# Performance work log

Measured on AMD Instinct MI355X. Metric: run time of the kernel, lower is better.

## Reference

```python
import jax, jax.numpy as jnp
import numpy as np
import math

B, H, S, D = 4, 16, 2048, 64

def setup_inputs() -> dict:
    key = jax.random.key(0)
    kq, kk, kv = jax.random.split(key, 3)
    Q = jax.random.normal(kq, (B, H, S, D), dtype=jnp.float32)
    K = jax.random.normal(kk, (B, H, S, D), dtype=jnp.float32)
    V = jax.random.normal(kv, (B, H, S, D), dtype=jnp.float32)
    # causal mask, broadcast to [B, H, S, S] as the module expects '... queries keys'
    causal = jnp.tril(jnp.ones((S, S), dtype=bool))
    mask = jnp.broadcast_to(causal, (B, H, S, S))
    return {"Q": Q, "K": K, "V": V, "mask": mask}

def reference(Q, K, V, mask):
    d_k = Q.shape[-1]
    # [B,H,S_q,S_k] scores
    qk = jnp.einsum('bhqd,bhkd->bhqk', Q, K) / math.sqrt(d_k)
    qk = jnp.where(mask, qk, -jnp.inf)
    sm = jax.nn.softmax(qk, axis=-1)
    return jnp.einsum('bhqk,bhkd->bhqd', sm, V)
```

## Files before the change

### kernel.cpp

```cpp
#include <hip/hip_runtime.h>

#define SEQ  2048
#define DH   64
#define QBLK 128
#define KBLK 64
#define NQB  (SEQ/QBLK)
#define NTIL (SEQ/KBLK)
#define THR  11.5f
#define KPAT(r) ((((r)&3)) + 8*((r)>>2))
#define WS_NEEDED ((size_t)2 * 64 * SEQ * DH * 2)

typedef short bf16x8 __attribute__((ext_vector_type(8)));
typedef float f32x16 __attribute__((ext_vector_type(16)));

union V4U { unsigned int w[4]; bf16x8 v; };

__device__ __forceinline__ short bfbits(float f) {
    unsigned int u = __float_as_uint(f);
    u += 0x7fff + ((u >> 16) & 1);
    return (short)(u >> 16);
}
__device__ __forceinline__ unsigned int cvtpk(float lo, float hi) {
    unsigned int r;
    asm("v_cvt_pk_bf16_f32 %0, %1, %2" : "=v"(r) : "v"(lo), "v"(hi));
    return r;
}
__device__ __forceinline__ int swz(int row, int col) {
    return row * 64 + (col ^ ((row & 7) << 3));
}
__device__ __forceinline__ void gload16(const void* g, void* l) {
    __builtin_amdgcn_global_load_lds(
        (const __attribute__((address_space(1))) unsigned int*)g,
        (__attribute__((address_space(3))) unsigned int*)l,
        16, 0, 0);
}

__global__ __launch_bounds__(256) void prep_kv(const float* __restrict__ Kg,
                                               const float* __restrict__ Vg,
                                               short* __restrict__ Kimg,
                                               short* __restrict__ Vimg) {
    __shared__ __align__(16) short Vt[64 * 64];
    const int tid = threadIdx.x;
    const int t   = blockIdx.x & (NTIL - 1);
    const int bh  = blockIdx.x / NTIL;
    const int kb  = t * KBLK;

    const float* Kb = Kg + (size_t)bh * SEQ * DH;
    const float* Vb = Vg + (size_t)bh * SEQ * DH;
    short* kim = Kimg + ((size_t)bh * NTIL + t) * 4096;
    short* vim = Vimg + ((size_t)bh * NTIL + t) * 4096;

    {
        const int kr = tid >> 2, sd0 = (tid & 3) * 16;
        const float* src = Kb + (size_t)(kb + kr) * DH + sd0;
        const float4 a0 = *reinterpret_cast<const float4*>(src);
        const float4 a1 = *reinterpret_cast<const float4*>(src + 4);
        const float4 a2 = *reinterpret_cast<const float4*>(src + 8);
        const float4 a3 = *reinterpret_cast<const float4*>(src + 12);
        V4U u0, u1;
        u0.w[0] = cvtpk(a0.x, a0.y); u0.w[1] = cvtpk(a0.z, a0.w);
        u0.w[2] = cvtpk(a1.x, a1.y); u0.w[3] = cvtpk(a1.z, a1.w);
        u1.w[0] = cvtpk(a2.x, a2.y); u1.w[1] = cvtpk(a2.z, a2.w);
        u1.w[2] = cvtpk(a3.x, a3.y); u1.w[3] = cvtpk(a3.z, a3.w);
        *reinterpret_cast<bf16x8*>(&kim[swz(kr, sd0)])     = u0.v;
        *reinterpret_cast<bf16x8*>(&kim[swz(kr, sd0 + 8)]) = u1.v;
    }
    {
        const int vk = tid & 63, vd0 = (tid >> 6) * 16;
        const float* src = Vb + (size_t)(kb + vk) * DH + vd0;
        const float4 b0 = *reinterpret_cast<const float4*>(src);
        const float4 b1 = *reinterpret_cast<const float4*>(src + 4);
        const float4 b2 = *reinterpret_cast<const float4*>(src + 8);
        const float4 b3 = *reinterpret_cast<const float4*>(src + 12);
        const float vv[16] = {b0.x,b0.y,b0.z,b0.w, b1.x,b1.y,b1.z,b1.w,
                              b2.x,b2.y,b2.z,b2.w, b3.x,b3.y,b3.z,b3.w};
        #pragma unroll
        for (int i = 0; i < 16; ++i)
            Vt[swz(vd0 + i, vk)] = bfbits(vv[i]);
    }
    __syncthreads();
    *reinterpret_cast<bf16x8*>(&vim[tid * 16])     = *reinterpret_cast<const bf16x8*>(&Vt[tid * 16]);
    *reinterpret_cast<bf16x8*>(&vim[tid * 16 + 8]) = *reinterpret_cast<const bf16x8*>(&Vt[tid * 16 + 8]);
}

__device__ __forceinline__ void load_kf8(const short* __restrict__ Ksb, int ql, int h,
                                         bf16x8 (&kf)[8]) {
    #pragma unroll
    for (int dc = 0; dc < 4; ++dc) {
        kf[dc]     = *reinterpret_cast<const bf16x8*>(&Ksb[swz(ql,      dc * 16 + h * 8)]);
        kf[4 + dc] = *reinterpret_cast<const bf16x8*>(&Ksb[swz(32 + ql, dc * 16 + h * 8)]);
    }
}
__device__ __forceinline__ void load_vf8(const short* __restrict__ Vtb, int ql, int h,
                                         bf16x8 (&vf)[8]) {
    #pragma unroll
    for (int kt = 0; kt < 4; ++kt) {
        vf[kt]     = *reinterpret_cast<const bf16x8*>(&Vtb[swz(ql,      kt * 16 + h * 8)]);
        vf[4 + kt] = *reinterpret_cast<const bf16x8*>(&Vtb[swz(32 + ql, kt * 16 + h * 8)]);
    }
}
__device__ __forceinline__ void qk_phase(const bf16x8 (&kf)[8], const bf16x8 (&qb)[4],
                                         f32x16& s0, f32x16& s1, bool v2) {
    #pragma unroll
    for (int i = 0; i < 16; ++i) s0[i] = 0.f;
    __builtin_amdgcn_s_setprio(1);
    #pragma unroll
    for (int dc = 0; dc < 4; ++dc)
        s0 = __builtin_amdgcn_mfma_f32_32x32x16_bf16(kf[dc], qb[dc], s0, 0, 0, 0);
    __builtin_amdgcn_s_setprio(0);
    if (v2) {
        #pragma unroll
        for (int i = 0; i < 16; ++i) s1[i] = 0.f;
        __builtin_amdgcn_s_setprio(1);
        #pragma unroll
        for (int dc = 0; dc < 4; ++dc)
            s1 = __builtin_amdgcn_mfma_f32_32x32x16_bf16(kf[4 + dc], qb[dc], s1, 0, 0, 0);
        __builtin_amdgcn_s_setprio(0);
    }
}
__device__ __forceinline__ void sm_pack(f32x16& s0, f32x16& s1, bool v2,
                                        int kb, int qw, int q, int h,
                                        float& m, float& lsum,
                                        f32x16& o0, f32x16& o1, bf16x8 (&pa)[4]) {
    if (kb + 31 > qw) {
        #pragma unroll
        for (int r = 0; r < 16; ++r)
            if (kb + KPAT(r) + 4 * h > q) s0[r] = -1e30f;
    }
    if (v2 && (kb + 63 > qw)) {
        #pragma unroll
        for (int r = 0; r < 16; ++r)
            if (kb + 32 + KPAT(r) + 4 * h > q) s1[r] = -1e30f;
    }
    float mx = s0[0];
    #pragma unroll
    for (int r = 1; r < 16; ++r) mx = fmaxf(mx, s0[r]);
    if (v2) {
        #pragma unroll
        for (int r = 0; r < 16; ++r) mx = fmaxf(mx, s1[r]);
    }
    if (!__all(mx <= m + THR)) {
        mx = fmaxf(mx, __shfl_xor(mx, 32));
        const float mn  = fmaxf(m, mx);
        const float scl = __builtin_amdgcn_exp2f(m - mn);
        m = mn;
        lsum *= scl;
        #pragma unroll
        for (int r = 0; r < 16; ++r) {
            const float sr = __shfl(scl, KPAT(r) + 4 * h);
            o0[r] *= sr; o1[r] *= sr;
        }
    }
    #pragma unroll
    for (int r = 0; r < 16; ++r) { s0[r] = __builtin_amdgcn_exp2f(s0[r] - m); lsum += s0[r]; }
    #pragma unroll
    for (int oct = 0; oct < 2; ++oct) {
        const unsigned int A0 = cvtpk(s0[oct*8+0], s0[oct*8+1]);
        const unsigned int A1 = cvtpk(s0[oct*8+2], s0[oct*8+3]);
        const unsigned int B0 = cvtpk(s0[oct*8+4], s0[oct*8+5]);
        const unsigned int B1 = cvtpk(s0[oct*8+6], s0[oct*8+7]);
        const unsigned int t0 = h ? A0 : B0, t1 = h ? A1 : B1;
        const unsigned int r0 = (unsigned int)__shfl_xor((int)t0, 32);
        const unsigned int r1 = (unsigned int)__shfl_xor((int)t1, 32);
        V4U u;
        u.w[0] = h ? r0 : A0; u.w[1] = h ? r1 : A1;
        u.w[2] = h ? B0 : r0; u.w[3] = h ? B1 : r1;
        pa[oct] = u.v;
    }
    if (v2) {
        #pragma unroll
        for (int r = 0; r < 16; ++r) { s1[r] = __builtin_amdgcn_exp2f(s1[r] - m); lsum += s1[r]; }
        #pragma unroll
        for (int oct = 0; oct < 2; ++oct) {
            const unsigned int A0 = cvtpk(s1[oct*8+0], s1[oct*8+1]);
            const unsigned int A1 = cvtpk(s1[oct*8+2], s1[oct*8+3]);
            const unsigned int B0 = cvtpk(s1[oct*8+4], s1[oct*8+5]);
            const unsigned int B1 = cvtpk(s1[oct*8+6], s1[oct*8+7]);
            const unsigned int t0 = h ? A0 : B0, t1 = h ? A1 : B1;
            const unsigned int r0 = (unsigned int)__shfl_xor((int)t0, 32);
            const unsigned int r1 = (unsigned int)__shfl_xor((int)t1, 32);
            V4U u;
            u.w[0] = h ? r0 : A0; u.w[1] = h ? r1 : A1;
            u.w[2] = h ? B0 : r0; u.w[3] = h ? B1 : r1;
            pa[2 + oct] = u.v;
        }
    }
}
__device__ __forceinline__ void pv_phase(const bf16x8 (&pa)[4], const bf16x8 (&vf)[8],
                                         f32x16& o0, f32x16& o1, bool v2) {
    __builtin_amdgcn_s_setprio(1);
    #pragma unroll
    for (int kt = 0; kt < 2; ++kt) {
        o0 = __builtin_amdgcn_mfma_f32_32x32x16_bf16(pa[kt], vf[kt],     o0, 0, 0, 0);
        o1 = __builtin_amdgcn_mfma_f32_32x32x16_bf16(pa[kt], vf[4 + kt], o1, 0, 0, 0);
    }
    if (v2) {
        #pragma unroll
        for (int kt = 2; kt < 4; ++kt) {
            o0 = __builtin_amdgcn_mfma_f32_32x32x16_bf16(pa[kt], vf[kt],     o0, 0, 0, 0);
            o1 = __builtin_amdgcn_mfma_f32_32x32x16_bf16(pa[kt], vf[4 + kt], o1, 0, 0, 0);
        }
    }
    __builtin_amdgcn_s_setprio(0);
}

__device__ __forceinline__ void load_qfrags(const float* Qb, int q, int h, float SC,
                                            bf16x8 (&qb)[4]) {
    const float* qp = Qb + (size_t)q * DH + h * 8;
    #pragma unroll
    for (int dc = 0; dc < 4; ++dc) {
        const float4 a = *reinterpret_cast<const float4*>(qp + dc * 16);
        const float4 b = *reinterpret_cast<const float4*>(qp + dc * 16 + 4);
        V4U u;
        u.w[0] = cvtpk(a.x * SC, a.y * SC);
        u.w[1] = cvtpk(a.z * SC, a.w * SC);
        u.w[2] = cvtpk(b.x * SC, b.y * SC);
        u.w[3] = cvtpk(b.z * SC, b.w * SC);
        qb[dc] = u.v;
    }
}

__device__ __forceinline__ void epilogue_store(float* Ob, int qw, int h, int ql,
                                               const f32x16& o0, const f32x16& o1,
                                               float lsum) {
    lsum += __shfl_xor(lsum, 32);
    const float inv = 1.0f / lsum;
    #pragma unroll
    for (int r = 0; r < 16; ++r) {
        const float ir  = __shfl(inv, KPAT(r) + 4 * h);
        const size_t row = (size_t)(qw + KPAT(r) + 4 * h);
        Ob[row * DH + ql]      = o0[r] * ir;
        Ob[row * DH + 32 + ql] = o1[r] * ir;
    }
}

#define STAGE(b_, t_) do {                                                   \
    const short* kim_ = kimg + (size_t)(t_) * 4096 + w * 1024 + lane * 8;    \
    const short* vim_ = vimg + (size_t)(t_) * 4096 + w * 1024 + lane * 8;    \
    gload16(kim_,       &Ks[b_][w * 1024]);                                  \
    gload16(kim_ + 512, &Ks[b_][w * 1024 + 512]);                            \
    gload16(vim_,       &Vt[b_][w * 1024]);                                  \
    gload16(vim_ + 512, &Vt[b_][w * 1024 + 512]);                            \
} while (0)

__global__ __launch_bounds__(256, 2) void attn_fwd(const float* __restrict__ Qg,
                                                   const short* __restrict__ Kimg,
                                                   const short* __restrict__ Vimg,
                                                   float* __restrict__ Og) {
    __shared__ __align__(16) short Ks[3][64 * 64];
    __shared__ __align__(16) short Vt[3][64 * 64];

    const int tid  = threadIdx.x;
    const int w    = tid >> 6;
    const int lane = tid & 63;
    const int h    = lane >> 5;
    const int ql   = lane & 31;

    const int p   = blockIdx.x & 7;
    const int bh  = blockIdx.x >> 3;
    const int qblkA = p, qblkB = NQB - 1 - p;

    const float* Qb   = Qg + (size_t)bh * SEQ * DH;
    const short* kimg = Kimg + (size_t)bh * NTIL * 4096;
    const short* vimg = Vimg + (size_t)bh * NTIL * 4096;
    float*       Ob   = Og + (size_t)bh * SEQ * DH;

    const float SC = 0.125f * 1.44269504f;

    const int qwA = qblkA * QBLK + w * 32, qA = qwA + ql, kendA = qwA + 32;
    const int qwB = qblkB * QBLK + w * 32, qB = qwB + ql, kendB = qwB + 32;
    const int nt  = qblkB * 2 + 2;

    STAGE(0, 0);
    STAGE(1, 1);

    bf16x8 qbA[4], qbB[4];
    load_qfrags(Qb, qA, h, SC, qbA);
    load_qfrags(Qb, qB, h, SC, qbB);

    f32x16 oA0, oA1, oB0, oB1;
    #pragma unroll
    for (int i = 0; i < 16; ++i) { oA0[i]=0.f; oA1[i]=0.f; oB0[i]=0.f; oB1[i]=0.f; }
    float mA = -1e30f, lA = 0.f, mB = -1e30f, lB = 0.f;

    __syncthreads();

    for (int t = 0; t < nt; ++t) {
        const int kb  = t * KBLK;
        const int cur = t % 3;

        if (t + 1 < nt) asm volatile("s_waitcnt vmcnt(4)" ::: "memory");
        else            asm volatile("s_waitcnt vmcnt(0)" ::: "memory");
        __builtin_amdgcn_s_barrier();

        if (t + 2 < nt) STAGE((t + 2) % 3, t + 2);

        const short* Ksb = &Ks[cur][0];
        const short* Vtb = &Vt[cur][0];
        const bool aAct = kb < kendA;
        const bool bAct = kb < kendB;
        const bool v2A  = kb + 32 < kendA;
        const bool v2B  = kb + 32 < kendB;

        bf16x8 kf[8];
        load_kf8(Ksb, ql, h, kf);

        f32x16 sA0, sA1, sB0, sB1;
        if (aAct) qk_phase(kf, qbA, sA0, sA1, v2A);
        if (bAct) qk_phase(kf, qbB, sB0, sB1, v2B);

        bf16x8 vf[8];
        load_vf8(Vtb, ql, h, vf);

        if (aAct) {
            bf16x8 paA[4];
            sm_pack(sA0, sA1, v2A, kb, qwA, qA, h, mA, lA, oA0, oA1, paA);
            pv_phase(paA, vf, oA0, oA1, v2A);
        }
        if (bAct) {
            bf16x8 paB[4];
            sm_pack(sB0, sB1, v2B, kb, qwB, qB, h, mB, lB, oB0, oB1, paB);
            pv_phase(paB, vf, oB0, oB1, v2B);
        }
    }

    epilogue_store(Ob, qwA, h, ql, oA0, oA1, lA);
    epilogue_store(Ob, qwB, h, ql, oB0, oB1, lB);
}

#define LOAD_STAGE(kb_) do {                                               \
    const float* ksrc = Kb + (size_t)((kb_) + skr) * DH + sd0;             \
    kr0 = *reinterpret_cast<const float4*>(ksrc);                          \
    kr1 = *reinterpret_cast<const float4*>(ksrc + 4);                      \
    kr2 = *reinterpret_cast<const float4*>(ksrc + 8);                      \
    kr3 = *reinterpret_cast<const float4*>(ksrc + 12);                     \
    const float* vsrc = Vb + (size_t)((kb_) + svk) * DH + svd0;            \
    vr0 = *reinterpret_cast<const float4*>(vsrc);                          \
    vr1 = *reinterpret_cast<const float4*>(vsrc + 4);                      \
    vr2 = *reinterpret_cast<const float4*>(vsrc + 8);                      \
    vr3 = *reinterpret_cast<const float4*>(vsrc + 12);                     \
} while (0)

#define CVT_WRITE(b_) do {                                                 \
    V4U u0, u1;                                                            \
    u0.w[0] = cvtpk(kr0.x, kr0.y); u0.w[1] = cvtpk(kr0.z, kr0.w);          \
    u0.w[2] = cvtpk(kr1.x, kr1.y); u0.w[3] = cvtpk(kr1.z, kr1.w);          \
    u1.w[0] = cvtpk(kr2.x, kr2.y); u1.w[1] = cvtpk(kr2.z, kr2.w);          \
    u1.w[2] = cvtpk(kr3.x, kr3.y); u1.w[3] = cvtpk(kr3.z, kr3.w);          \
    *reinterpret_cast<bf16x8*>(&Ks[b_][swz(skr, sd0)])     = u0.v;         \
    *reinterpret_cast<bf16x8*>(&Ks[b_][swz(skr, sd0 + 8)]) = u1.v;         \
    const float vv[16] = {vr0.x,vr0.y,vr0.z,vr0.w, vr1.x,vr1.y,vr1.z,vr1.w,\
                          vr2.x,vr2.y,vr2.z,vr2.w, vr3.x,vr3.y,vr3.z,vr3.w};\
    _Pragma("unroll")                                                      \
    for (int i_ = 0; i_ < 16; ++i_)                                        \
        Vt[b_][swz(svd0 + i_, svk)] = bfbits(vv[i_]);                      \
} while (0)

__global__ __launch_bounds__(256) void attn_fwd_fb(const float* __restrict__ Qg,
                                                   const float* __restrict__ Kg,
                                                   const float* __restrict__ Vg,
                                                   float* __restrict__ Og) {
    __shared__ __align__(16) short Ks[2][64 * 64];
    __shared__ __align__(16) short Vt[2][64 * 64];

    const int tid  = threadIdx.x;
    const int w    = tid >> 6;
    const int lane = tid & 63;
    const int h    = lane >> 5;
    const int ql   = lane & 31;

    const int j    = blockIdx.x & (NQB - 1);
    const int bh   = blockIdx.x / NQB;
    const int qblk = ((bh >> 4) & 1) ? (NQB - 1 - j) : j;
    const int q0   = qblk * QBLK;
    const int qw   = q0 + w * 32;
    const int q    = qw + ql;

    const float* Qb = Qg + (size_t)bh * SEQ * DH;
    const float* Kb = Kg + (size_t)bh * SEQ * DH;
    const float* Vb = Vg + (size_t)bh * SEQ * DH;
    float*       Ob = Og + (size_t)bh * SEQ * DH;

    const float SC = 0.125f * 1.44269504f;

    const int skr  = tid >> 2;
    const int sd0  = (tid & 3) * 16;
    const int svk  = tid & 63;
    const int svd0 = (tid >> 6) * 16;

    float4 kr0, kr1, kr2, kr3, vr0, vr1, vr2, vr3;
    LOAD_STAGE(0);

    bf16x8 qb[4];
    load_qfrags(Qb, q, h, SC, qb);

    f32x16 o0, o1;
    #pragma unroll
    for (int i = 0; i < 16; ++i) { o0[i] = 0.f; o1[i] = 0.f; }
    float m = -1e30f, lsum = 0.f;

    CVT_WRITE(0);
    __syncthreads();

    const int kend = qw + 32;
    const int nt   = (q0 + QBLK) / KBLK;

    for (int t = 0; t < nt; ++t) {
        const int kb  = t * KBLK;
        const int cur = t & 1;
        if (t + 1 < nt) LOAD_STAGE(kb + KBLK);

        if (kb < kend) {
            const bool v2 = (kb + 32 < kend);
            bf16x8 kf[8];
            load_kf8(&Ks[cur][0], ql, h, kf);
            f32x16 s0, s1;
            qk_phase(kf, qb, s0, s1, v2);
            bf16x8 vf[8];
            load_vf8(&Vt[cur][0], ql, h, vf);
            bf16x8 pa[4];
            sm_pack(s0, s1, v2, kb, qw, q, h, m, lsum, o0, o1, pa);
            pv_phase(pa, vf, o0, o1, v2);
        }
        if (t + 1 < nt) CVT_WRITE(cur ^ 1);
        __syncthreads();
    }

    epilogue_store(Ob, qw, h, ql, o0, o1, lsum);
}

extern "C" void kernel_launch(void* const* d_in, const int* in_sizes, int n_in,
                              void* d_out, int out_size, void* d_ws, size_t ws_size,
                              hipStream_t stream) {
    const float* Q = (const float*)d_in[0];
    const float* K = (const float*)d_in[1];
    const float* V = (const float*)d_in[2];
    float* O = (float*)d_out;

    if (ws_size >= WS_NEEDED) {
        short* Kimg = (short*)d_ws;
        short* Vimg = Kimg + (size_t)64 * NTIL * 4096;
        prep_kv<<<dim3(64 * NTIL), 256, 0, stream>>>(K, V, Kimg, Vimg);
        attn_fwd<<<dim3(64 * (NQB / 2)), 256, 0, stream>>>(Q, Kimg, Vimg, O);
    } else {
        attn_fwd_fb<<<dim3(64 * NQB), 256, 0, stream>>>(Q, K, V, O);
    }
}
```

Measured before the change: 86.09 us.

## Split paired query blocks across 8 waves instead of 4 waves each handling two

Before, each of the 4 waves handled two query blocks (A and B); now the block has 512 threads and waves 0-3 take query block A while waves 4-7 take block B. Each wave keeps one set of accumulators, which lowers register pressure and doubles the waves available to hide latency. K and V fragments are now read from LDS inside the QK and PV helpers rather than preloaded, and tile staging is split across 8 waves with a matching vmcnt. The block-to-query-pair mapping is rotated by bh to spread causal work imbalance. In exchange, each K/V fragment is read from LDS once per wave for a single query block, so LDS traffic per useful MFMA roughly doubles. Waves in the A half also sit idle at barriers once their causal range is done.

Result: slower. 116.1 us (+34.8%).

```diff
diff --git a/kernel.cpp b/kernel.cpp
--- a/kernel.cpp
+++ b/kernel.cpp
@@ -83,41 +83,39 @@
     *reinterpret_cast<bf16x8*>(&vim[tid * 16 + 8]) = *reinterpret_cast<const bf16x8*>(&Vt[tid * 16 + 8]);
 }
 
-__device__ __forceinline__ void load_kf8(const short* __restrict__ Ksb, int ql, int h,
-                                         bf16x8 (&kf)[8]) {
+__device__ __forceinline__ void load_qfrags(const float* Qb, int q, int h, float SC,
+                                            bf16x8 (&qb)[4]) {
+    const float* qp = Qb + (size_t)q * DH + h * 8;
     #pragma unroll
     for (int dc = 0; dc < 4; ++dc) {
-        kf[dc]     = *reinterpret_cast<const bf16x8*>(&Ksb[swz(ql,      dc * 16 + h * 8)]);
-        kf[4 + dc] = *reinterpret_cast<const bf16x8*>(&Ksb[swz(32 + ql, dc * 16 + h * 8)]);
-    }
-}
-__device__ __forceinline__ void load_vf8(const short* __restrict__ Vtb, int ql, int h,
-                                         bf16x8 (&vf)[8]) {
-    #pragma unroll
-    for (int kt = 0; kt < 4; ++kt) {
-        vf[kt]     = *reinterpret_cast<const bf16x8*>(&Vtb[swz(ql,      kt * 16 + h * 8)]);
-        vf[4 + kt] = *reinterpret_cast<const bf16x8*>(&Vtb[swz(32 + ql, kt * 16 + h * 8)]);
-    }
-}
-__device__ __forceinline__ void qk_phase(const bf16x8 (&kf)[8], const bf16x8 (&qb)[4],
-                                         f32x16& s0, f32x16& s1, bool v2) {
-    #pragma unroll
-    for (int i = 0; i < 16; ++i) s0[i] = 0.f;
+        const float4 a = *reinterpret_cast<const float4*>(qp + dc * 16);
+        const float4 b = *reinterpret_cast<const float4*>(qp + dc * 16 + 4);
+        V4U u;
+        u.w[0] = cvtpk(a.x * SC, a.y * SC);
+        u.w[1] = cvtpk(a.z * SC, a.w * SC);
+        u.w[2] = cvtpk(b.x * SC, b.y * SC);
+        u.w[3] = cvtpk(b.z * SC, b.w * SC);
+        qb[dc] = u.v;
+    }
+}
+
+__device__ __forceinline__ f32x16 qk32(const short* __restrict__ Ksb, int row, int ql, int h,
+                                       const bf16x8 (&qb)[4]) {
+    f32x16 s;
+    #pragma unroll
+    for (int i = 0; i < 16; ++i) s[i] = 0.f;
+    bf16x8 kf[4];
+    #pragma unroll
+    for (int dc = 0; dc < 4; ++dc)
+        kf[dc] = *reinterpret_cast<const bf16x8*>(&Ksb[swz(row + ql, dc * 16 + h * 8)]);
     __builtin_amdgcn_s_setprio(1);
     #pragma unroll
     for (int dc = 0; dc < 4; ++dc)
-        s0 = __builtin_amdgcn_mfma_f32_32x32x16_bf16(kf[dc], qb[dc], s0, 0, 0, 0);
+        s = __builtin_amdgcn_mfma_f32_32x32x16_bf16(kf[dc], qb[dc], s, 0, 0, 0);
     __builtin_amdgcn_s_setprio(0);
-    if (v2) {
-        #pragma unroll
-        for (int i = 0; i < 16; ++i) s1[i] = 0.f;
-        __builtin_amdgcn_s_setprio(1);
-        #pragma unroll
-        for (int dc = 0; dc < 4; ++dc)
-            s1 = __builtin_amdgcn_mfma_f32_32x32x16_bf16(kf[4 + dc], qb[dc], s1, 0, 0, 0);
-        __builtin_amdgcn_s_setprio(0);
-    }
-}
+    return s;
+}
+
 __device__ __forceinline__ void sm_pack(f32x16& s0, f32x16& s1, bool v2,
                                         int kb, int qw, int q, int h,
                                         float& m, float& lsum,
@@ -186,38 +184,23 @@
         }
     }
 }
-__device__ __forceinline__ void pv_phase(const bf16x8 (&pa)[4], const bf16x8 (&vf)[8],
-                                         f32x16& o0, f32x16& o1, bool v2) {
+
+__device__ __forceinline__ void pv_half(const short* __restrict__ Vtb, int drow, int ql, int h,
+                                        const bf16x8 (&pa)[4], f32x16& o, bool v2) {
     __builtin_amdgcn_s_setprio(1);
     #pragma unroll
     for (int kt = 0; kt < 2; ++kt) {
-        o0 = __builtin_amdgcn_mfma_f32_32x32x16_bf16(pa[kt], vf[kt],     o0, 0, 0, 0);
-        o1 = __builtin_amdgcn_mfma_f32_32x32x16_bf16(pa[kt], vf[4 + kt], o1, 0, 0, 0);
+        const bf16x8 vf = *reinterpret_cast<const bf16x8*>(&Vtb[swz(drow + ql, kt * 16 + h * 8)]);
+        o = __builtin_amdgcn_mfma_f32_32x32x16_bf16(pa[kt], vf, o, 0, 0, 0);
     }
     if (v2) {
         #pragma unroll
         for (int kt = 2; kt < 4; ++kt) {
-            o0 = __builtin_amdgcn_mfma_f32_32x32x16_bf16(pa[kt], vf[kt],     o0, 0, 0, 0);
-            o1 = __builtin_amdgcn_mfma_f32_32x32x16_bf16(pa[kt], vf[4 + kt], o1, 0, 0, 0);
+            const bf16x8 vf = *reinterpret_cast<const bf16x8*>(&Vtb[swz(drow + ql, kt * 16 + h * 8)]);
+            o = __builtin_amdgcn_mfma_f32_32x32x16_bf16(pa[kt], vf, o, 0, 0, 0);
         }
     }
     __builtin_amdgcn_s_setprio(0);
-}
-
-__device__ __forceinline__ void load_qfrags(const float* Qb, int q, int h, float SC,
-                                            bf16x8 (&qb)[4]) {
-    const float* qp = Qb + (size_t)q * DH + h * 8;
-    #pragma unroll
-    for (int dc = 0; dc < 4; ++dc) {
-        const float4 a = *reinterpret_cast<const float4*>(qp + dc * 16);
-        const float4 b = *reinterpret_cast<const float4*>(qp + dc * 16 + 4);
-        V4U u;
-        u.w[0] = cvtpk(a.x * SC, a.y * SC);
-        u.w[1] = cvtpk(a.z * SC, a.w * SC);
-        u.w[2] = cvtpk(b.x * SC, b.y * SC);
-        u.w[3] = cvtpk(b.z * SC, b.w * SC);
-        qb[dc] = u.v;
-    }
 }
 
 __device__ __forceinline__ void epilogue_store(float* Ob, int qw, int h, int ql,
@@ -235,15 +218,13 @@
 }
 
 #define STAGE(b_, t_) do {                                                   \
-    const short* kim_ = kimg + (size_t)(t_) * 4096 + w * 1024 + lane * 8;    \
-    const short* vim_ = vimg + (size_t)(t_) * 4096 + w * 1024 + lane * 8;    \
-    gload16(kim_,       &Ks[b_][w * 1024]);                                  \
-    gload16(kim_ + 512, &Ks[b_][w * 1024 + 512]);                            \
-    gload16(vim_,       &Vt[b_][w * 1024]);                                  \
-    gload16(vim_ + 512, &Vt[b_][w * 1024 + 512]);                            \
+    const short* kim_ = kimg + (size_t)(t_) * 4096 + w * 512 + lane * 8;     \
+    const short* vim_ = vimg + (size_t)(t_) * 4096 + w * 512 + lane * 8;     \
+    gload16(kim_, &Ks[b_][w * 512]);                                         \
+    gload16(vim_, &Vt[b_][w * 512]);                                         \
 } while (0)
 
-__global__ __launch_bounds__(256, 2) void attn_fwd(const float* __restrict__ Qg,
+__global__ __launch_bounds__(512, 2) void attn_fwd(const float* __restrict__ Qg,
                                                    const short* __restrict__ Kimg,
                                                    const short* __restrict__ Vimg,
                                                    float* __restrict__ Og) {
@@ -255,10 +236,14 @@
     const int lane = tid & 63;
     const int h    = lane >> 5;
     const int ql   = lane & 31;
-
-    const int p   = blockIdx.x & 7;
+    const int wq   = w & 3;
+    const int isB  = w >> 2;
+
+    const int j   = blockIdx.x & 7;
     const int bh  = blockIdx.x >> 3;
-    const int qblkA = p, qblkB = NQB - 1 - p;
+    const int pp  = (j + bh) & 7;
+    const int qblkA = pp, qblkB = NQB - 1 - pp;
+    const int qblk  = isB ? qblkB : qblkA;
 
     const float* Qb   = Qg + (size_t)bh * SEQ * DH;
     const short* kimg = Kimg + (size_t)bh * NTIL * 4096;
@@ -267,21 +252,21 @@
 
     const float SC = 0.125f * 1.44269504f;
 
-    const int qwA = qblkA * QBLK + w * 32, qA = qwA + ql, kendA = qwA + 32;
-    const int qwB = qblkB * QBLK + w * 32, qB = qwB + ql, kendB = qwB + 32;
-    const int nt  = qblkB * 2 + 2;
+    const int qw   = qblk * QBLK + wq * 32;
+    const int q    = qw + ql;
+    const int kend = qw + 32;
+    const int nt   = qblkB * 2 + 2;
 
     STAGE(0, 0);
     STAGE(1, 1);
 
-    bf16x8 qbA[4], qbB[4];
-    load_qfrags(Qb, qA, h, SC, qbA);
-    load_qfrags(Qb, qB, h, SC, qbB);
-
-    f32x16 oA0, oA1, oB0, oB1;
-    #pragma unroll
-    for (int i = 0; i < 16; ++i) { oA0[i]=0.f; oA1[i]=0.f; oB0[i]=0.f; oB1[i]=0.f; }
-    float mA = -1e30f, lA = 0.f, mB = -1e30f, lB = 0.f;
+    bf16x8 qb[4];
+    load_qfrags(Qb, q, h, SC, qb);
+
+    f32x16 o0, o1;
+    #pragma unroll
+    for (int i = 0; i < 16; ++i) { o0[i] = 0.f; o1[i] = 0.f; }
+    float m = -1e30f, lsum = 0.f;
 
     __syncthreads();
 
@@ -289,43 +274,30 @@
         const int kb  = t * KBLK;
         const int cur = t % 3;
 
-        if (t + 1 < nt) asm volatile("s_waitcnt vmcnt(4)" ::: "memory");
+        if (t + 1 < nt) asm volatile("s_waitcnt vmcnt(2)" ::: "memory");
         else            asm volatile("s_waitcnt vmcnt(0)" ::: "memory");
         __builtin_amdgcn_s_barrier();
 
         if (t + 2 < nt) STAGE((t + 2) % 3, t + 2);
 
-        const short* Ksb = &Ks[cur][0];
-        const short* Vtb = &Vt[cur][0];
-        const bool aAct = kb < kendA;
-        const bool bAct = kb < kendB;
-        const bool v2A  = kb + 32 < kendA;
-        const bool v2B  = kb + 32 < kendB;
-
-        bf16x8 kf[8];
-        load_kf8(Ksb, ql, h, kf);
-
-        f32x16 sA0, sA1, sB0, sB1;
-        if (aAct) qk_phase(kf, qbA, sA0, sA1, v2A);
-        if (bAct) qk_phase(kf, qbB, sB0, sB1, v2B);
-
-        bf16x8 vf[8];
-        load_vf8(Vtb, ql, h, vf);
-
-        if (aAct) {
-            bf16x8 paA[4];
-            sm_pack(sA0, sA1, v2A, kb, qwA, qA, h, mA, lA, oA0, oA1, paA);
-            pv_phase(paA, vf, oA0, oA1, v2A);
+        if (kb < kend) {
+            const bool v2 = (kb + 32 < kend);
+            const short* Ksb = &Ks[cur][0];
+            const short* Vtb = &Vt[cur][0];
+
+            f32x16 s0 = qk32(Ksb, 0, ql, h, qb);
+            f32x16 s1;
+            if (v2) s1 = qk32(Ksb, 32, ql, h, qb);
+
+            bf16x8 pa[4];
+            sm_pack(s0, s1, v2, kb, qw, q, h, m, lsum, o0, o1, pa);
+
+            pv_half(Vtb, 0,  ql, h, pa, o0, v2);
+            pv_half(Vtb, 32, ql, h, pa, o1, v2);
         }
-        if (bAct) {
-            bf16x8 paB[4];
-            sm_pack(sB0, sB1, v2B, kb, qwB, qB, h, mB, lB, oB0, oB1, paB);
-            pv_phase(paB, vf, oB0, oB1, v2B);
-        }
-    }
-
-    epilogue_store(Ob, qwA, h, ql, oA0, oA1, lA);
-    epilogue_store(Ob, qwB, h, ql, oB0, oB1, lB);
+    }
+
+    epilogue_store(Ob, qw, h, ql, o0, o1, lsum);
 }
 
 #define LOAD_STAGE(kb_) do {                                               \
@@ -412,15 +384,13 @@
 
         if (kb < kend) {
             const bool v2 = (kb + 32 < kend);
-            bf16x8 kf[8];
-            load_kf8(&Ks[cur][0], ql, h, kf);
-            f32x16 s0, s1;
-            qk_phase(kf, qb, s0, s1, v2);
-            bf16x8 vf[8];
-            load_vf8(&Vt[cur][0], ql, h, vf);
+            f32x16 s0 = qk32(&Ks[cur][0], 0, ql, h, qb);
+            f32x16 s1;
+            if (v2) s1 = qk32(&Ks[cur][0], 32, ql, h, qb);
             bf16x8 pa[4];
             sm_pack(s0, s1, v2, kb, qw, q, h, m, lsum, o0, o1, pa);
-            pv_phase(pa, vf, o0, o1, v2);
+            pv_half(&Vt[cur][0], 0,  ql, h, pa, o0, v2);
+            pv_half(&Vt[cur][0], 32, ql, h, pa, o1, v2);
         }
         if (t + 1 < nt) CVT_WRITE(cur ^ 1);
         __syncthreads();
@@ -441,7 +411,7 @@
         short* Kimg = (short*)d_ws;
         short* Vimg = Kimg + (size_t)64 * NTIL * 4096;
         prep_kv<<<dim3(64 * NTIL), 256, 0, stream>>>(K, V, Kimg, Vimg);
-        attn_fwd<<<dim3(64 * (NQB / 2)), 256, 0, stream>>>(Q, Kimg, Vimg, O);
+        attn_fwd<<<dim3(64 * (NQB / 2)), 512, 0, stream>>>(Q, Kimg, Vimg, O);
     } else {
         attn_fwd_fb<<<dim3(64 * NQB), 256, 0, stream>>>(Q, K, V, O);
     }
```
